# Kernel tuning notes

Measured on AMD Instinct MI355X. Metric: run time of the kernel, lower is better.

The kernel has to match this reference:

```python
import jax, jax.numpy as jnp
import numpy as np

B_SZ, SEQ, D_IN = 8, 4096, 1024
STATE, HEADS = 1024, 16
HEAD_DIM = STATE // HEADS
LN_EPS = 1e-5


def setup_inputs() -> dict:
    key = jax.random.key(0)
    ks = jax.random.split(key, 10)
    inp = {
        "x": jax.random.normal(ks[0], (B_SZ, SEQ, D_IN), dtype=jnp.float32),
        "W_in": jax.random.normal(ks[1], (STATE, D_IN), dtype=jnp.float32) * (1.0 / np.sqrt(D_IN)),
        "b_in": jnp.zeros((STATE,), dtype=jnp.float32),
        "log_A": jax.random.normal(ks[2], (HEADS, HEAD_DIM), dtype=jnp.float32) * 0.1 + 0.1,
        "B_p": jax.random.normal(ks[3], (HEADS, HEAD_DIM), dtype=jnp.float32) * 0.1 + 0.1,
        "C_p": jax.random.normal(ks[4], (HEADS, HEAD_DIM), dtype=jnp.float32) * 0.1 + 0.1,
        "W_out": jax.random.normal(ks[5], (STATE, STATE), dtype=jnp.float32) * (1.0 / np.sqrt(STATE)),
        "b_out": jnp.zeros((STATE,), dtype=jnp.float32),
        "gamma": jnp.ones((STATE,), dtype=jnp.float32),
        "beta": jnp.zeros((STATE,), dtype=jnp.float32),
    }
    return inp


def reference(x, W_in, b_in, log_A, B_p, C_p, W_out, b_out, gamma, beta):
    Bsz, S, _ = x.shape
    H, Dh = log_A.shape
    # input projection: (B,S,state)
    h = jnp.einsum("bsd,ed->bse", x, W_in) + b_in
    h = h.reshape(Bsz, S, H, Dh)
    decay = jnp.exp(-jax.nn.softplus(log_A))  # (H,Dh), time-invariant

    def step(s, xt):  # s,xt: (B,H,Dh)
        s = s * decay + B_p * xt
        return s, C_p * s

    s0 = jnp.zeros((Bsz, H, Dh), dtype=h.dtype)
    _, ys = jax.lax.scan(step, s0, jnp.swapaxes(h, 0, 1))  # ys: (S,B,H,Dh)
    y = jnp.swapaxes(ys, 0, 1).reshape(Bsz, S, H * Dh)
    out = jnp.einsum("bse,fe->bsf", y, W_out) + b_out
    # dropout in eval mode = identity; layer norm over last dim
    mu = out.mean(-1, keepdims=True)
    var = out.var(-1, keepdims=True)
    return (out - mu) * jax.lax.rsqrt(var + LN_EPS) * gamma + beta
```

## Files before the change

### kernel.cpp

```cpp
#include <hip/hip_runtime.h>

#define B_SZ  8
#define SEQ   4096
#define D_IN  1024
#define STATE 1024
#define M_TOT (B_SZ * SEQ)
#define LN_EPS 1e-5f
#define GK    1024
#define GN    1024

#define SCAN_L 128
#define SCAN_W 64

typedef short short8_t __attribute__((ext_vector_type(8)));
typedef float f32x4 __attribute__((ext_vector_type(4)));

__device__ __forceinline__ unsigned short f2bf(float f) {
  union { float f; unsigned u; } v; v.f = f;
  unsigned r = v.u + 0x7fffu + ((v.u >> 16) & 1u);
  return (unsigned short)(r >> 16);
}
__device__ __forceinline__ float bf2f(unsigned short h) {
  union { unsigned u; float f; } v; v.u = ((unsigned)h) << 16;
  return v.f;
}

__device__ __forceinline__ void gload16(const void* g, void* l) {
  __builtin_amdgcn_global_load_lds(
      (const __attribute__((address_space(1))) void*)g,
      (__attribute__((address_space(3))) void*)l, 16, 0, 0);
}

#define BAR()    __builtin_amdgcn_s_barrier()
#define SCHED0() __builtin_amdgcn_sched_barrier(0)

__global__ __launch_bounds__(256) void cast_kernel(const float* __restrict__ in,
                                                   unsigned short* __restrict__ out,
                                                   int n4) {
  int i = blockIdx.x * 256 + threadIdx.x;
  if (i < n4) {
    float4 v = ((const float4*)in)[i];
    ushort4 o;
    o.x = f2bf(v.x); o.y = f2bf(v.y); o.z = f2bf(v.z); o.w = f2bf(v.w);
    ((ushort4*)out)[i] = o;
  }
}


__device__ __forceinline__ void stage(const char* gbase, char* dbase, int t, int q) {
  gload16(gbase + (q * 131072 + t * 128), dbase + q * 8192);
}

template <int H>
__device__ __forceinline__ void readA(const char* pk0, const char* pk1,
                                      short8_t (&a)[4][2]) {
#pragma unroll
  for (int mf = 0; mf < 4; mf++) {
    a[mf][0] = *(const short8_t*)(pk0 + ((H * 64 + mf * 16) << 7));
    a[mf][1] = *(const short8_t*)(pk1 + ((H * 64 + mf * 16) << 7));
  }
}
template <int NH>
__device__ __forceinline__ void readB(const char* pk0, const char* pk1,
                                      short8_t (&b)[2][2]) {
#pragma unroll
  for (int nf = 0; nf < 2; nf++) {
    b[nf][0] = *(const short8_t*)(pk0 + ((NH * 32 + nf * 16) << 7));
    b[nf][1] = *(const short8_t*)(pk1 + ((NH * 32 + nf * 16) << 7));
  }
}

template <int H, int NH>
__device__ __forceinline__ void mfma16(short8_t (&a)[4][2], short8_t (&b)[2][2],
                                       f32x4 (&acc)[8][4]) {
  __builtin_amdgcn_s_setprio(1);
#pragma unroll
  for (int ks = 0; ks < 2; ks++)
#pragma unroll
    for (int mf = 0; mf < 4; mf++)
#pragma unroll
      for (int nf = 0; nf < 2; nf++)
        acc[H * 4 + mf][NH * 2 + nf] = __builtin_amdgcn_mfma_f32_16x16x32_bf16(
            a[mf][ks], b[nf][ks], acc[H * 4 + mf][NH * 2 + nf], 0, 0, 0);
  __builtin_amdgcn_s_setprio(0);
}

__global__ __launch_bounds__(512, 2) void gemm256(
    const unsigned short* __restrict__ A,
    const unsigned short* __restrict__ Bt,
    const float* __restrict__ bias,
    unsigned short* __restrict__ C,
    int M) {
  __shared__ __attribute__((aligned(16))) unsigned short As[2][256 * 64];
  __shared__ __attribute__((aligned(16))) unsigned short Bs[2][256 * 64];

  const int tid = threadIdx.x;
  const int w = tid >> 6, lane = tid & 63;
  const int wm = w >> 2, wn = w & 3;
  const int fr = lane & 15;
  const int fkb = (lane >> 4) * 16;

  const int nwg = gridDim.x;
  const int cpx = nwg >> 3;
  const int bid = blockIdx.x;
  const int wg = (bid & 7) * cpx + (bid >> 3);
  const int nbx = GN >> 8;
  const long m0 = (long)(wg / nbx) * 256;
  const long n0 = (long)(wg % nbx) * 256;

  const int xorv = (fr & 7) << 4;
  const int lo0 = (fr * 128 + 0  + fkb) ^ xorv;
  const int lo1 = (fr * 128 + 64 + fkb) ^ xorv;
  const char* pA0k0 = (const char*)&As[0][0] + wm * 16384 + lo0;
  const char* pA0k1 = (const char*)&As[0][0] + wm * 16384 + lo1;
  const char* pA1k0 = (const char*)&As[1][0] + wm * 16384 + lo0;
  const char* pA1k1 = (const char*)&As[1][0] + wm * 16384 + lo1;
  const char* pB0k0 = (const char*)&Bs[0][0] + wn * 8192 + lo0;
  const char* pB0k1 = (const char*)&Bs[0][0] + wn * 8192 + lo1;
  const char* pB1k0 = (const char*)&Bs[1][0] + wn * 8192 + lo0;
  const char* pB1k1 = (const char*)&Bs[1][0] + wn * 8192 + lo1;

  const int srow = tid >> 3;
  const int c2 = ((tid & 7) * 16) ^ ((srow & 7) << 4);
  const char* gA0 = (const char*)(A  + (m0 + srow) * (long)GK) + c2;
  const char* gB0 = (const char*)(Bt + (n0 + srow) * (long)GK) + c2;
  char* dA0 = (char*)&As[0][0] + ((tid >> 6) << 10);
  char* dA1 = (char*)&As[1][0] + ((tid >> 6) << 10);
  char* dB0 = (char*)&Bs[0][0] + ((tid >> 6) << 10);
  char* dB1 = (char*)&Bs[1][0] + ((tid >> 6) << 10);

  short8_t aE[4][2], aO[4][2], b0[2][2], b1[2][2], b2[2][2];
  f32x4 acc[8][4] = {};

  const int nit = (GK >> 6) >> 1;

#pragma unroll
  for (int q = 0; q < 4; q++) stage(gA0, dA0, 0, q);
#pragma unroll
  for (int q = 0; q < 4; q++) stage(gB0, dB0, 0, q);
#pragma unroll
  for (int q = 0; q < 4; q++) stage(gA0, dA1, 1, q);
  SCHED0();
  asm volatile("s_waitcnt vmcnt(4)" ::: "memory");
  BAR();
  readA<0>(pA0k0, pA0k1, aE);
  readB<0>(pB0k0, pB0k1, b0);

#pragma unroll 1
  for (int i = 0; i < nit; ++i) {
    const bool last = (i == nit - 1);
    const int t1 = 2 * i + 1, t2 = 2 * i + 2, t3 = 2 * i + 3;

    readB<1>(pB0k0, pB0k1, b1);
#pragma unroll
    for (int q = 0; q < 4; q++) stage(gB0, dB1, t1, q);
    SCHED0();
    mfma16<0, 0>(aE, b0, acc);
    BAR();

    readA<1>(pA0k0, pA0k1, aO);
    SCHED0();
    mfma16<0, 1>(aE, b1, acc);
    BAR();

    readB<0>(pB0k0, pB0k1, b2);
    SCHED0();
    mfma16<1, 1>(aO, b1, acc);
    asm volatile("s_waitcnt vmcnt(0)" ::: "memory");
    BAR();

    readA<0>(pA1k0, pA1k1, aE);
    readB<0>(pB1k0, pB1k1, b0);
    if (!last) {
#pragma unroll
      for (int q = 0; q < 4; q++) stage(gA0, dA0, t2, q);
    }
    SCHED0();
    mfma16<1, 0>(aO, b2, acc);
    BAR();

    readB<1>(pB1k0, pB1k1, b1);
    if (!last) {
#pragma unroll
      for (int q = 0; q < 4; q++) stage(gB0, dB0, t2, q);
    }
    SCHED0();
    mfma16<0, 0>(aE, b0, acc);
    BAR();

    readA<1>(pA1k0, pA1k1, aO);
    SCHED0();
    mfma16<0, 1>(aE, b1, acc);
    BAR();

    readB<0>(pB1k0, pB1k1, b2);
    SCHED0();
    mfma16<1, 1>(aO, b1, acc);
    if (!last) {
      asm volatile("s_waitcnt vmcnt(0)" ::: "memory");
    }
    BAR();

    if (!last) {
      readA<0>(pA0k0, pA0k1, aE);
      readB<0>(pB0k0, pB0k1, b0);
#pragma unroll
      for (int q = 0; q < 4; q++) stage(gA0, dA1, t3, q);
    }
    SCHED0();
    mfma16<1, 0>(aO, b2, acc);
    BAR();
  }

  const int cc = lane & 15;
  const int cr = (lane >> 4) * 4;
  char* epi = (w < 4) ? ((char*)&As[0][0] + w * 16384)
                      : ((char*)&Bs[0][0] + (w - 4) * 16384);
  float bv[4];
#pragma unroll
  for (int nf = 0; nf < 4; nf++) bv[nf] = bias[n0 + wn * 64 + nf * 16 + cc];
#pragma unroll
  for (int mf = 0; mf < 8; mf++) {
#pragma unroll
    for (int r = 0; r < 4; r++) {
      const int row = mf * 16 + cr + r;
      const int rx = (row & 7) << 4;
#pragma unroll
      for (int nf = 0; nf < 4; nf++) {
        const int off = (row * 128 + (nf * 16 + cc) * 2) ^ rx;
        *(unsigned short*)(epi + off) = f2bf(acc[mf][nf][r] + bv[nf]);
      }
    }
  }
  const int rr = lane >> 3;
  const int rdoff = (lane * 16) ^ ((rr & 7) << 4);
  char* cbase = (char*)C + (m0 + wm * 128) * (GN * 2) + n0 * 2 + wn * 128 + (lane & 7) * 16;
#pragma unroll
  for (int s = 0; s < 16; s++) {
    short8_t vv = *(const short8_t*)(epi + s * 1024 + rdoff);
    *(short8_t*)(cbase + (long)(s * 8 + rr) * (GN * 2)) = vv;
  }
}

__global__ __launch_bounds__(256) void scan_kernel(
    const unsigned short* __restrict__ h,
    const float* __restrict__ log_A,
    const float* __restrict__ Bp,
    const float* __restrict__ Cp,
    unsigned short* __restrict__ y) {
  const int e = blockIdx.x * 256 + threadIdx.x;
  const int chunk = blockIdx.y;
  const int b = blockIdx.z;
  const float la = log_A[e];
  const float d = expf(-log1pf(expf(la)));
  const float bp = Bp[e];
  const float cp = Cp[e];
  const long base = ((long)b * SEQ) * STATE + e;
  const int t0 = chunk * SCAN_L;
  const int tw = (t0 >= SCAN_W) ? (t0 - SCAN_W) : 0;
  float s = 0.f;
  for (int t = tw; t < t0; ++t)
    s = fmaf(s, d, bp * bf2f(h[base + (long)t * STATE]));
  for (int t = t0; t < t0 + SCAN_L; ++t) {
    s = fmaf(s, d, bp * bf2f(h[base + (long)t * STATE]));
    y[base + (long)t * STATE] = f2bf(cp * s);
  }
}

__global__ __launch_bounds__(256) void ln_kernel(
    const unsigned short* __restrict__ X,
    const float* __restrict__ gamma,
    const float* __restrict__ beta,
    float* __restrict__ out) {
  const int row = blockIdx.x;
  const int tid = threadIdx.x;
  const long base = (long)row * STATE;
  ushort4 v = *(const ushort4*)&X[base + tid * 4];
  float x0 = bf2f(v.x), x1 = bf2f(v.y), x2 = bf2f(v.z), x3 = bf2f(v.w);
  float s = x0 + x1 + x2 + x3;
  float q = x0 * x0 + x1 * x1 + x2 * x2 + x3 * x3;
#pragma unroll
  for (int o = 32; o > 0; o >>= 1) {
    s += __shfl_xor(s, o);
    q += __shfl_xor(q, o);
  }
  __shared__ float sw[4], qw[4];
  const int wave = tid >> 6, lane = tid & 63;
  if (lane == 0) { sw[wave] = s; qw[wave] = q; }
  __syncthreads();
  s = sw[0] + sw[1] + sw[2] + sw[3];
  q = qw[0] + qw[1] + qw[2] + qw[3];
  const float mu = s * (1.0f / STATE);
  const float var = q * (1.0f / STATE) - mu * mu;
  const float inv = rsqrtf(var + LN_EPS);
  const int c = tid * 4;
  float4 o;
  o.x = (x0 - mu) * inv * gamma[c + 0] + beta[c + 0];
  o.y = (x1 - mu) * inv * gamma[c + 1] + beta[c + 1];
  o.z = (x2 - mu) * inv * gamma[c + 2] + beta[c + 2];
  o.w = (x3 - mu) * inv * gamma[c + 3] + beta[c + 3];
  *(float4*)&out[base + tid * 4] = o;
}

extern "C" void kernel_launch(void* const* d_in, const int* in_sizes, int n_in,
                              void* d_out, int out_size, void* d_ws, size_t ws_size,
                              hipStream_t stream) {
  const float* x     = (const float*)d_in[0];
  const float* W_in  = (const float*)d_in[1];
  const float* b_in  = (const float*)d_in[2];
  const float* log_A = (const float*)d_in[3];
  const float* Bp    = (const float*)d_in[4];
  const float* Cp    = (const float*)d_in[5];
  const float* W_out = (const float*)d_in[6];
  const float* b_out = (const float*)d_in[7];
  const float* gamma = (const float*)d_in[8];
  const float* beta  = (const float*)d_in[9];
  float* out = (float*)d_out;

  char* ws = (char*)d_ws;
  unsigned short* Wi_b = (unsigned short*)(ws);
  unsigned short* Wo_b = (unsigned short*)(ws + (2ull << 20));
  unsigned short* xb   = (unsigned short*)(ws + (4ull << 20));
  unsigned short* hb   = (unsigned short*)(ws + (68ull << 20));

  cast_kernel<<<(M_TOT * D_IN / 4) / 256, 256, 0, stream>>>(x, xb, M_TOT * D_IN / 4);
  cast_kernel<<<(STATE * D_IN / 4) / 256, 256, 0, stream>>>(W_in, Wi_b, STATE * D_IN / 4);
  cast_kernel<<<(STATE * STATE / 4) / 256, 256, 0, stream>>>(W_out, Wo_b, STATE * STATE / 4);

  gemm256<<<dim3((GN / 256) * (M_TOT / 256)), 512, 0, stream>>>(
      xb, Wi_b, b_in, hb, M_TOT);

  scan_kernel<<<dim3(STATE / 256, SEQ / SCAN_L, B_SZ), 256, 0, stream>>>(
      hb, log_A, Bp, Cp, xb);

  gemm256<<<dim3((GN / 256) * (M_TOT / 256)), 512, 0, stream>>>(
      xb, Wo_b, b_out, hb, M_TOT);

  ln_kernel<<<M_TOT, 256, 0, stream>>>(hb, gamma, beta, out);
}
```

Baseline: 266.9 us.

## Restructure GEMM main loop to spread global staging across sub-steps

Rewrites the software-pipelined GEMM main loop so that global-to-LDS staging is split into pairs of loads spread over all four MFMA sub-steps, with partial vmcnt waits instead of full drains. It also drops the b2 register fragment and reorders the MFMA sub-tiles so B fragments are reused. The aim is smoother overlap of memory traffic with MFMA work and lower register pressure. In exchange it adds extra barriers per sub-step, which may cost synchronization time.

```diff
diff --git a/kernel.cpp b/kernel.cpp
--- a/kernel.cpp
+++ b/kernel.cpp
@@ -129,7 +129,7 @@
   char* dB0 = (char*)&Bs[0][0] + ((tid >> 6) << 10);
   char* dB1 = (char*)&Bs[1][0] + ((tid >> 6) << 10);
 
-  short8_t aE[4][2], aO[4][2], b0[2][2], b1[2][2], b2[2][2];
+  short8_t aE[4][2], aO[4][2], b0[2][2], b1[2][2];
   f32x4 acc[8][4] = {};
 
   const int nit = (GK >> 6) >> 1;
@@ -138,77 +138,86 @@
   for (int q = 0; q < 4; q++) stage(gA0, dA0, 0, q);
 #pragma unroll
   for (int q = 0; q < 4; q++) stage(gB0, dB0, 0, q);
-#pragma unroll
-  for (int q = 0; q < 4; q++) stage(gA0, dA1, 1, q);
+  stage(gA0, dA1, 1, 0);
+  stage(gA0, dA1, 1, 1);
   SCHED0();
-  asm volatile("s_waitcnt vmcnt(4)" ::: "memory");
+  asm volatile("s_waitcnt vmcnt(2)" ::: "memory");
   BAR();
-  readA<0>(pA0k0, pA0k1, aE);
-  readB<0>(pB0k0, pB0k1, b0);
 
 #pragma unroll 1
   for (int i = 0; i < nit; ++i) {
     const bool last = (i == nit - 1);
     const int t1 = 2 * i + 1, t2 = 2 * i + 2, t3 = 2 * i + 3;
 
+    readA<0>(pA0k0, pA0k1, aE);
+    readB<0>(pB0k0, pB0k1, b0);
+    stage(gA0, dA1, t1, 2);
+    stage(gA0, dA1, t1, 3);
+    SCHED0(); BAR();
+    mfma16<0, 0>(aE, b0, acc);
+    SCHED0(); BAR();
+
     readB<1>(pB0k0, pB0k1, b1);
-#pragma unroll
-    for (int q = 0; q < 4; q++) stage(gB0, dB1, t1, q);
+    stage(gB0, dB1, t1, 0);
+    stage(gB0, dB1, t1, 1);
+    SCHED0(); BAR();
+    mfma16<0, 1>(aE, b1, acc);
+    SCHED0(); BAR();
+
+    readA<1>(pA0k0, pA0k1, aO);
+    stage(gB0, dB1, t1, 2);
+    stage(gB0, dB1, t1, 3);
+    SCHED0(); BAR();
+    mfma16<1, 0>(aO, b0, acc);
+    SCHED0(); BAR();
+
+    if (!last) {
+      stage(gA0, dA0, t2, 0);
+      stage(gA0, dA0, t2, 1);
+    }
+    SCHED0(); BAR();
+    mfma16<1, 1>(aO, b1, acc);
     SCHED0();
-    mfma16<0, 0>(aE, b0, acc);
-    BAR();
-
-    readA<1>(pA0k0, pA0k1, aO);
-    SCHED0();
-    mfma16<0, 1>(aE, b1, acc);
-    BAR();
-
-    readB<0>(pB0k0, pB0k1, b2);
-    SCHED0();
-    mfma16<1, 1>(aO, b1, acc);
-    asm volatile("s_waitcnt vmcnt(0)" ::: "memory");
+    if (last) { asm volatile("s_waitcnt vmcnt(0)" ::: "memory"); }
+    else      { asm volatile("s_waitcnt vmcnt(2)" ::: "memory"); }
     BAR();
 
     readA<0>(pA1k0, pA1k1, aE);
     readB<0>(pB1k0, pB1k1, b0);
     if (!last) {
-#pragma unroll
-      for (int q = 0; q < 4; q++) stage(gA0, dA0, t2, q);
-    }
+      stage(gA0, dA0, t2, 2);
+      stage(gA0, dA0, t2, 3);
+    }
+    SCHED0(); BAR();
+    mfma16<0, 0>(aE, b0, acc);
+    SCHED0(); BAR();
+
+    readB<1>(pB1k0, pB1k1, b1);
+    if (!last) {
+      stage(gB0, dB0, t2, 0);
+      stage(gB0, dB0, t2, 1);
+    }
+    SCHED0(); BAR();
+    mfma16<0, 1>(aE, b1, acc);
+    SCHED0(); BAR();
+
+    readA<1>(pA1k0, pA1k1, aO);
+    if (!last) {
+      stage(gB0, dB0, t2, 2);
+      stage(gB0, dB0, t2, 3);
+    }
+    SCHED0(); BAR();
+    mfma16<1, 0>(aO, b0, acc);
+    SCHED0(); BAR();
+
+    if (!last) {
+      stage(gA0, dA1, t3, 0);
+      stage(gA0, dA1, t3, 1);
+    }
+    SCHED0(); BAR();
+    mfma16<1, 1>(aO, b1, acc);
     SCHED0();
-    mfma16<1, 0>(aO, b2, acc);
-    BAR();
-
-    readB<1>(pB1k0, pB1k1, b1);
-    if (!last) {
-#pragma unroll
-      for (int q = 0; q < 4; q++) stage(gB0, dB0, t2, q);
-    }
-    SCHED0();
-    mfma16<0, 0>(aE, b0, acc);
-    BAR();
-
-    readA<1>(pA1k0, pA1k1, aO);
-    SCHED0();
-    mfma16<0, 1>(aE, b1, acc);
-    BAR();
-
-    readB<0>(pB1k0, pB1k1, b2);
-    SCHED0();
-    mfma16<1, 1>(aO, b1, acc);
-    if (!last) {
-      asm volatile("s_waitcnt vmcnt(0)" ::: "memory");
-    }
-    BAR();
-
-    if (!last) {
-      readA<0>(pA0k0, pA0k1, aE);
-      readB<0>(pB0k0, pB0k1, b0);
-#pragma unroll
-      for (int q = 0; q < 4; q++) stage(gA0, dA1, t3, q);
-    }
-    SCHED0();
-    mfma16<1, 0>(aO, b2, acc);
+    if (!last) { asm volatile("s_waitcnt vmcnt(2)" ::: "memory"); }
     BAR();
   }
 
```

Measured after the change: 259.2 us. -2.9%, faster.
